# Performance work log

Measured on AMD Instinct MI355X. Metric: run time of the kernel, lower is better.

## Reference

```python
import jax, jax.numpy as jnp
import numpy as np

EPS = 1e-8

def setup_inputs() -> dict:
    key = jax.random.key(0)
    k1, k2 = jax.random.split(key)
    B, IN, OUT, G = 32768, 256, 256, 5
    x = jax.random.normal(k1, (B, IN), dtype=jnp.float32)
    grid = jnp.linspace(-1.0, 1.0, G).astype(jnp.float32)
    coef = jax.random.normal(k2, (OUT, IN, G), dtype=jnp.float32) * 0.1
    scale = jnp.ones((OUT, IN), dtype=jnp.float32)
    bias = jnp.zeros((OUT,), dtype=jnp.float32)
    return {"x": x, "grid": grid, "coef": coef, "scale": scale, "bias": bias}

def reference(x, grid, coef, scale, bias):
    # global min-max normalization to [-1, 1]
    xmin, xmax = x.min(), x.max()
    xn = 2.0 * (x - xmin) / (xmax - xmin + EPS) - 1.0
    # cubic bump B-spline-like basis: (batch, in, grid)
    dist = jnp.abs(xn[..., None] - grid)
    basis = jnp.where(dist < 1.0, 1.0 - dist ** 3, 0.0)
    basis = basis / (basis.sum(axis=-1, keepdims=True) + EPS)
    # fused contraction over (in, grid); equals ((basis*coef).sum(-1)*scale).sum(-1)
    w = coef * scale[..., None]          # (out, in, grid)
    out = jnp.einsum('big,oig->bo', basis, w) + bias
    return out
```

## Files before the change

### kernel.cpp

```cpp
#include <hip/hip_runtime.h>
#include <stdint.h>


#define B_SZ   32768
#define IN_SZ  256
#define OUT_SZ 256
#define EPSF   1e-8f

typedef __bf16 bf16x8 __attribute__((ext_vector_type(8)));
typedef unsigned short ushort8 __attribute__((ext_vector_type(8)));
typedef float floatx16 __attribute__((ext_vector_type(16)));
typedef float float2v __attribute__((ext_vector_type(2)));

__device__ __forceinline__ unsigned short f2bf(float f) {
  unsigned u = __float_as_uint(f);
  u += 0x7FFFu + ((u >> 16) & 1u);
  return (unsigned short)(u >> 16);
}


__global__ void __launch_bounds__(256) prep_kernel(const float* __restrict__ coef,
                                                   const float* __restrict__ scale,
                                                   const float* __restrict__ x,
                                                   unsigned short* __restrict__ wf,
                                                   float* __restrict__ part, int n4) {
  const int t = threadIdx.x;
  if (blockIdx.x < 256) {
    int idx = blockIdx.x * 256 + t;
    int o = idx >> 8, i = idx & 255;
    float s = scale[idx];
    const float* c = coef + (size_t)idx * 5;
    ushort8 v;
    v[0] = f2bf(c[0] * s); v[1] = f2bf(c[1] * s); v[2] = f2bf(c[2] * s);
    v[3] = f2bf(c[3] * s); v[4] = f2bf(c[4] * s);
    v[5] = 0; v[6] = 0; v[7] = 0;
    int chunk = (((o >> 5) * 64 + (i >> 2)) * 2 + ((i >> 1) & 1)) * 64
                + (i & 1) * 32 + (o & 31);
    *(ushort8*)(wf + (size_t)chunk * 8) = v;
  } else {
    int mb = blockIdx.x - 256;
    const float4* x4 = (const float4*)x;
    float lmin = 1e30f, lmax = -1e30f;
    for (int i = mb * 256 + t; i < n4; i += 256 * 256) {
      float4 v = x4[i];
      lmin = fminf(lmin, fminf(fminf(v.x, v.y), fminf(v.z, v.w)));
      lmax = fmaxf(lmax, fmaxf(fmaxf(v.x, v.y), fmaxf(v.z, v.w)));
    }
    #pragma unroll
    for (int off = 32; off >= 1; off >>= 1) {
      lmin = fminf(lmin, __shfl_down(lmin, off, 64));
      lmax = fmaxf(lmax, __shfl_down(lmax, off, 64));
    }
    __shared__ float smn[4], smx[4];
    if ((t & 63) == 0) { smn[t >> 6] = lmin; smx[t >> 6] = lmax; }
    __syncthreads();
    if (t == 0) {
      part[2 * mb]     = fminf(fminf(smn[0], smn[1]), fminf(smn[2], smn[3]));
      part[2 * mb + 1] = fmaxf(fmaxf(smx[0], smx[1]), fmaxf(smx[2], smx[3]));
    }
  }
}

__global__ void __launch_bounds__(256, 2) kan_gemm(
    const float* __restrict__ x,
    const unsigned short* __restrict__ wf,
    const float* __restrict__ bias,
    const float* __restrict__ part,
    float* __restrict__ out)
{
  __shared__ float2 red[4];

  const int t = threadIdx.x;
  const int lane = t & 63;
  const int wm = t >> 6;
  const int l31 = lane & 31, lh = lane >> 5;
  const int bRow = blockIdx.x * 128;
  const int bCol = blockIdx.y * 128;
  const int row = bRow + wm * 32 + l31;

  const unsigned short* bp[4];
  #pragma unroll
  for (int ni = 0; ni < 4; ++ni)
    bp[ni] = wf + (size_t)(blockIdx.y * 4 + ni) * 65536 + (size_t)lane * 8;
  const float* xp = x + (size_t)row * IN_SZ;

  bf16x8 bReg[2][2][4];
  float4 xq[2];
  #pragma unroll
  for (int u = 0; u < 2; ++u) {
    xq[u] = *(const float4*)(xp + u * 4);
    #pragma unroll
    for (int ks = 0; ks < 2; ++ks)
      #pragma unroll
      for (int ni = 0; ni < 4; ++ni)
        bReg[u][ks][ni] = *(const bf16x8*)(bp[ni] + u * 1024 + ks * 512);
  }
  xp += 8;
  #pragma unroll
  for (int ni = 0; ni < 4; ++ni) bp[ni] += 2048;

  float2 p = ((const float2*)part)[t];
  float mn = p.x, mx = p.y;
  #pragma unroll
  for (int off = 32; off >= 1; off >>= 1) {
    mn = fminf(mn, __shfl_down(mn, off, 64));
    mx = fmaxf(mx, __shfl_down(mx, off, 64));
  }
  if (lane == 0) red[wm] = make_float2(mn, mx);
  __syncthreads();
  mn = fminf(fminf(red[0].x, red[1].x), fminf(red[2].x, red[3].x));
  mx = fmaxf(fmaxf(red[0].y, red[1].y), fmaxf(red[2].y, red[3].y));
  const float scA = 2.0f / (mx - mn + EPSF);
  const float scB = -mn * scA - 1.0f;

  auto basisfrag = [&](float xval) -> bf16x8 {
    float xn = fmaf(xval, scA, scB);
    float2v xx = {xn, xn};
    float2v dA = xx + (float2v){1.0f, 0.5f};
    float2v dB = xx - (float2v){0.5f, 1.0f};
    float2v aA = __builtin_elementwise_max(dA, -dA);
    float2v aB = __builtin_elementwise_max(dB, -dB);
    float2v one2 = {1.0f, 1.0f};
    float2v z2 = {0.0f, 0.0f};
    float2v bA = __builtin_elementwise_max(one2 - dA * dA * aA, z2);
    float2v bB = __builtin_elementwise_max(one2 - dB * dB * aB, z2);
    float b2 = fmaxf(fmaf(xn * xn, -fabsf(xn), 1.0f), 0.0f);
    float sum = (bA.x + bA.y) + (bB.x + bB.y) + (b2 + EPSF);
    float inv = __builtin_amdgcn_rcpf(sum);
    float2v sA = bA * inv;
    float2v sB = bB * inv;
    bf16x8 av = {};
    av[0] = (__bf16)sA.x; av[1] = (__bf16)sA.y; av[2] = (__bf16)(b2 * inv);
    av[3] = (__bf16)sB.x; av[4] = (__bf16)sB.y;
    return av;
  };

  floatx16 acc[4] = {};

  for (int base = 0; base < 64; base += 2) {
    #pragma unroll
    for (int u = 0; u < 2; ++u) {
      const int kt = base + u;

      float xv0 = lh ? xq[u].y : xq[u].x;
      float xv1 = lh ? xq[u].w : xq[u].z;
      bf16x8 af0 = basisfrag(xv0);
      bf16x8 af1 = basisfrag(xv1);

      #pragma unroll
      for (int ni = 0; ni < 4; ++ni)
        acc[ni] = __builtin_amdgcn_mfma_f32_32x32x16_bf16(af0, bReg[u][0][ni], acc[ni], 0, 0, 0);
      #pragma unroll
      for (int ni = 0; ni < 4; ++ni)
        acc[ni] = __builtin_amdgcn_mfma_f32_32x32x16_bf16(af1, bReg[u][1][ni], acc[ni], 0, 0, 0);

      if (kt < 62) {
        xq[u] = *(const float4*)(xp + u * 4);
        #pragma unroll
        for (int ks = 0; ks < 2; ++ks)
          #pragma unroll
          for (int ni = 0; ni < 4; ++ni)
            bReg[u][ks][ni] = *(const bf16x8*)(bp[ni] + u * 1024 + ks * 512);
      }
    }
    xp += 8;
    #pragma unroll
    for (int ni = 0; ni < 4; ++ni) bp[ni] += 2048;
  }

  #pragma unroll
  for (int ni = 0; ni < 4; ++ni) {
    int o = bCol + ni * 32 + l31;
    float bs = bias[o];
    int rb = bRow + wm * 32 + 4 * lh;
    #pragma unroll
    for (int reg = 0; reg < 16; ++reg) {
      int r = rb + (reg & 3) + 8 * (reg >> 2);
      out[(size_t)r * OUT_SZ + o] = acc[ni][reg] + bs;
    }
  }
}

extern "C" void kernel_launch(void* const* d_in, const int* in_sizes, int n_in,
                              void* d_out, int out_size, void* d_ws, size_t ws_size,
                              hipStream_t stream) {
  const float* x     = (const float*)d_in[0];
  const float* coef  = (const float*)d_in[2];
  const float* scale = (const float*)d_in[3];
  const float* bias  = (const float*)d_in[4];
  float* out = (float*)d_out;

  size_t need = 4096 + (size_t)OUT_SZ * IN_SZ * 8 * 2;
  if (ws_size < need) return;

  float* part = (float*)d_ws;
  unsigned short* wf = (unsigned short*)((char*)d_ws + 4096);

  prep_kernel<<<512, 256, 0, stream>>>(coef, scale, x, wf, part,
                                       (B_SZ * IN_SZ) / 4);
  dim3 g(B_SZ / 128, OUT_SZ / 128);
  kan_gemm<<<g, 256, 0, stream>>>(x, wf, bias, part, out);
}
```

Before: 144.4 us.

## Stage weight fragments in double-buffered LDS via global_load_lds shared across waves

Before, each of the four waves in a block loaded the same bf16 weight fragments from global memory straight into registers, so each block fetched its B tile four times. Now each 16-step K chunk of weights is copied once per block into a double-buffered LDS tile using direct global-to-LDS loads, and the next chunk is prefetched while the current one is used. All waves read their MFMA B operands from LDS, and x values are prefetched a chunk ahead. This trades L2 traffic and register pressure for 64KB of LDS per block, a barrier per chunk, and extra LDS read bandwidth, which could limit occupancy.

Result: faster. 139.5 us (-3.4%).

```diff
diff --git a/kernel.cpp b/kernel.cpp
--- a/kernel.cpp
+++ b/kernel.cpp
@@ -68,6 +68,7 @@
     const float* __restrict__ part,
     float* __restrict__ out)
 {
+  __shared__ __align__(16) unsigned short Bb[2][16384];
   __shared__ float2 red[4];
 
   const int t = threadIdx.x;
@@ -78,26 +79,26 @@
   const int bCol = blockIdx.y * 128;
   const int row = bRow + wm * 32 + l31;
 
-  const unsigned short* bp[4];
+  auto stage = [&](int c, int buf) {
+    #pragma unroll
+    for (int r = 0; r < 8; ++r) {
+      int idx = r * 4 + wm;
+      const unsigned short* src = wf +
+          ((size_t)(((blockIdx.y * 4 + (idx >> 3)) * 64 + (c * 4 + ((idx >> 1) & 3))) * 2
+                    + (idx & 1))) * 512 + (size_t)lane * 8;
+      __builtin_amdgcn_global_load_lds(
+          (const __attribute__((address_space(1))) unsigned int*)src,
+          (__attribute__((address_space(3))) unsigned int*)(&Bb[buf][idx * 512 + lane * 8]),
+          16, 0, 0);
+    }
+  };
+
+  const float* xrow = x + (size_t)row * IN_SZ;
+
+  stage(0, 0);
+  float4 xq[4], xqn[4];
   #pragma unroll
-  for (int ni = 0; ni < 4; ++ni)
-    bp[ni] = wf + (size_t)(blockIdx.y * 4 + ni) * 65536 + (size_t)lane * 8;
-  const float* xp = x + (size_t)row * IN_SZ;
-
-  bf16x8 bReg[2][2][4];
-  float4 xq[2];
-  #pragma unroll
-  for (int u = 0; u < 2; ++u) {
-    xq[u] = *(const float4*)(xp + u * 4);
-    #pragma unroll
-    for (int ks = 0; ks < 2; ++ks)
-      #pragma unroll
-      for (int ni = 0; ni < 4; ++ni)
-        bReg[u][ks][ni] = *(const bf16x8*)(bp[ni] + u * 1024 + ks * 512);
-  }
-  xp += 8;
-  #pragma unroll
-  for (int ni = 0; ni < 4; ++ni) bp[ni] += 2048;
+  for (int g = 0; g < 4; ++g) xq[g] = *(const float4*)(xrow + g * 4);
 
   float2 p = ((const float2*)part)[t];
   float mn = p.x, mx = p.y;
@@ -137,35 +138,39 @@
 
   floatx16 acc[4] = {};
 
-  for (int base = 0; base < 64; base += 2) {
-    #pragma unroll
-    for (int u = 0; u < 2; ++u) {
-      const int kt = base + u;
-
-      float xv0 = lh ? xq[u].y : xq[u].x;
-      float xv1 = lh ? xq[u].w : xq[u].z;
+  for (int c = 0; c < 16; ++c) {
+    const int buf = c & 1;
+
+    __syncthreads();
+
+    if (c < 15) {
+      stage(c + 1, buf ^ 1);
+      #pragma unroll
+      for (int g = 0; g < 4; ++g)
+        xqn[g] = *(const float4*)(xrow + (c + 1) * 16 + g * 4);
+    }
+
+    #pragma unroll
+    for (int ktr = 0; ktr < 4; ++ktr) {
+      float xv0 = lh ? xq[ktr].y : xq[ktr].x;
+      float xv1 = lh ? xq[ktr].w : xq[ktr].z;
       bf16x8 af0 = basisfrag(xv0);
       bf16x8 af1 = basisfrag(xv1);
 
       #pragma unroll
-      for (int ni = 0; ni < 4; ++ni)
-        acc[ni] = __builtin_amdgcn_mfma_f32_32x32x16_bf16(af0, bReg[u][0][ni], acc[ni], 0, 0, 0);
+      for (int ni = 0; ni < 4; ++ni) {
+        bf16x8 b0 = *(const bf16x8*)(&Bb[buf][((ni * 4 + ktr) * 2 + 0) * 512 + lane * 8]);
+        acc[ni] = __builtin_amdgcn_mfma_f32_32x32x16_bf16(af0, b0, acc[ni], 0, 0, 0);
+      }
       #pragma unroll
-      for (int ni = 0; ni < 4; ++ni)
-        acc[ni] = __builtin_amdgcn_mfma_f32_32x32x16_bf16(af1, bReg[u][1][ni], acc[ni], 0, 0, 0);
-
-      if (kt < 62) {
-        xq[u] = *(const float4*)(xp + u * 4);
-        #pragma unroll
-        for (int ks = 0; ks < 2; ++ks)
-          #pragma unroll
-          for (int ni = 0; ni < 4; ++ni)
-            bReg[u][ks][ni] = *(const bf16x8*)(bp[ni] + u * 1024 + ks * 512);
+      for (int ni = 0; ni < 4; ++ni) {
+        bf16x8 b1 = *(const bf16x8*)(&Bb[buf][((ni * 4 + ktr) * 2 + 1) * 512 + lane * 8]);
+        acc[ni] = __builtin_amdgcn_mfma_f32_32x32x16_bf16(af1, b1, acc[ni], 0, 0, 0);
       }
     }
-    xp += 8;
-    #pragma unroll
-    for (int ni = 0; ni < 4; ++ni) bp[ni] += 2048;
+
+    #pragma unroll
+    for (int g = 0; g < 4; ++g) xq[g] = xqn[g];
   }
 
   #pragma unroll
```
